# Optimization experiments

Hardware: AMD Instinct MI355X
Metric: run time of the kernel (lower is better)

Reference implementation:

```python
import jax, jax.numpy as jnp
import numpy as np

N_NODES = 20000
N_EDGES = 640000
IN_DIM = 256
HID = 128
N_GRAPHS = 64


def setup_inputs() -> dict:
    key = jax.random.key(0)
    ks = jax.random.split(key, 9)
    x = jax.random.normal(ks[0], (N_NODES, IN_DIM), jnp.float32)
    edge_index = jax.random.randint(ks[1], (2, N_EDGES), 0, N_NODES, dtype=jnp.int32)
    batch = jnp.sort(jax.random.randint(ks[2], (N_NODES,), 0, N_GRAPHS, dtype=jnp.int32))

    def lin(k, fan_in, fan_out):
        # torch.nn.Linear default init: U(-1/sqrt(fan_in), 1/sqrt(fan_in))
        bound = 1.0 / np.sqrt(fan_in)
        kw, kb = jax.random.split(k)
        W = jax.random.uniform(kw, (fan_in, fan_out), jnp.float32, -bound, bound)
        b = jax.random.uniform(kb, (fan_out,), jnp.float32, -bound, bound)
        return W, b

    W0, b0 = lin(ks[3], IN_DIM, HID)
    W1, b1 = lin(ks[4], HID, HID)
    W2, b2 = lin(ks[5], HID, HID)
    return dict(x=x, edge_index=edge_index, batch=batch,
                W0=W0, b0=b0, W1=W1, b1=b1, W2=W2, b2=b2)


def reference(x, edge_index, batch, W0, b0, W1, b1, W2, b2):
    src, dst = edge_index[0], edge_index[1]
    edge_batch = batch[src]  # [E] segment id per edge
    ones = jnp.ones((edge_batch.shape[0], 1), x.dtype)
    counts = jax.ops.segment_sum(ones, edge_batch, num_segments=N_GRAPHS)
    inv_counts = 1.0 / jnp.maximum(counts, 1.0)

    def pool(z):
        # gather endpoint features, concat -> [E, 2*HID], mean pool by graph
        edge_emb = jnp.concatenate([z[src], z[dst]], axis=1)
        return jax.ops.segment_sum(edge_emb, edge_batch, num_segments=N_GRAPHS) * inv_counts

    g = []
    z = x
    for W, b in ((W0, b0), (W1, b1), (W2, b2)):
        z = z @ W + b
        g.append(pool(z))
    return jnp.concatenate(g, axis=1)  # [N_GRAPHS, 3 * 2 * HID]
```

## Files before the change

### kernel.cpp

```cpp
#include <hip/hip_runtime.h>

#define N_NODES 20000
#define N_EDGES 640000
#define N_GRAPHS 64

#define NCHUNK 128
#define CHUNK_SZ 157
#define GSPLIT 8
#define GSUB 8

#define BG_TILE 2048
#define NBG 313
#define SEGCAP 80
#define GR_CAP 768
#define NSLOT4 (NBG * SEGCAP / 4)

#define CD_OFF      0
#define DEG_OFF     1280000
#define CNT_OFF     1300000
#define Y_OFF       1300064
#define PART_OFF    1316448
#define BH_OFF      3413600
#define VALS_OFF    3433632

__global__ __launch_bounds__(256) void bucket_g_k(const int* __restrict__ ei,
                                                  const int* __restrict__ batch,
                                                  unsigned* __restrict__ vals,
                                                  unsigned* __restrict__ bh,
                                                  float* __restrict__ Y) {
    __shared__ unsigned hist[N_GRAPHS];
    __shared__ unsigned base[N_GRAPHS + 1];
    __shared__ unsigned lv[BG_TILE];
    const int t = threadIdx.x;
    const int blk = blockIdx.x;
    if (t < N_GRAPHS) hist[t] = 0u;
    __syncthreads();

    const int e0 = blk * BG_TILE;
    const int ecnt = (e0 + BG_TILE <= N_EDGES) ? BG_TILE : (N_EDGES - e0);
    unsigned pv[8], rnk[8], gg[8];
#pragma unroll
    for (int k = 0; k < 8; ++k) {
        int i = t + k * 256;
        if (i < ecnt) {
            unsigned s = (unsigned)ei[e0 + i];
            unsigned d = (unsigned)ei[N_EDGES + e0 + i];
            unsigned g = (unsigned)batch[s];
            pv[k] = (s << 15) | d;
            gg[k] = g;
            rnk[k] = atomicAdd(&hist[g], 1u);
        } else {
            gg[k] = 0xFFFFFFFFu;
        }
    }
    __syncthreads();
    if (t == 0) {
        unsigned acc = 0u;
        base[0] = 0u;
        for (int g = 0; g < N_GRAPHS; ++g) { acc += hist[g]; base[g + 1] = acc; }
    }
    if (t < N_GRAPHS) {
        unsigned c = hist[t];
        bh[blk * N_GRAPHS + t] = (c > SEGCAP) ? SEGCAP : c;
    }
    __syncthreads();
#pragma unroll
    for (int k = 0; k < 8; ++k) {
        if (gg[k] != 0xFFFFFFFFu) lv[base[gg[k]] + rnk[k]] = pv[k];
    }
    __syncthreads();
    for (int i = t; i < ecnt; i += 256) {
        int lo = 0, hi = N_GRAPHS - 1;
        while (lo < hi) { int m = (lo + hi + 1) >> 1; if (base[m] <= (unsigned)i) lo = m; else hi = m - 1; }
        unsigned slot = (unsigned)i - base[lo];
        if (slot < SEGCAP)
            vals[((size_t)lo * NBG + blk) * SEGCAP + slot] = lv[i];
    }
    if (blk == 0) {
        float4* y4 = (float4*)Y;
        for (int i = t; i < 64 * 64; i += 256) y4[i] = make_float4(0.f, 0.f, 0.f, 0.f);
    }
}

__global__ __launch_bounds__(1024) void cd_col_k(const unsigned* __restrict__ vals,
                                                 const unsigned* __restrict__ bh,
                                                 const int* __restrict__ batch,
                                                 float* __restrict__ Cdcol,
                                                 float* __restrict__ deg,
                                                 float* __restrict__ counts) {
    __shared__ unsigned scnt[NBG];
    __shared__ unsigned dh[2500];
    __shared__ unsigned sdeg[GR_CAP];
    __shared__ int s_lo, s_hi;
    const int t = threadIdx.x;
    const int g = blockIdx.x >> 2;
    const int q = blockIdx.x & 3;
    const int d0 = q * 5000;

    for (int i = t; i < 2500; i += 1024) dh[i] = 0u;
    if (t < NBG) scnt[t] = bh[t * N_GRAPHS + g];
    if (q == 0) {
        if (t < GR_CAP) sdeg[t] = 0u;
        if (t == 0) {
            int lo = 0, hi = N_NODES;
            while (lo < hi) { int m = (lo + hi) >> 1; if (batch[m] < g) lo = m + 1; else hi = m; }
            s_lo = lo;
            int lo2 = lo; hi = N_NODES;
            while (lo2 < hi) { int m = (lo2 + hi) >> 1; if (batch[m] < g + 1) lo2 = m + 1; else hi = m; }
            s_hi = lo2;
        }
    }
    __syncthreads();
    const int lo = (q == 0) ? s_lo : 0;

    const uint4* v4 = (const uint4*)(vals + (size_t)g * NBG * SEGCAP);
    for (int i = t; i < NSLOT4; i += 1024) {
        uint4 v = *(v4 + i);
        unsigned w = (unsigned)i * 4u;
        unsigned seg = (unsigned)(((unsigned long long)w * 53687092ull) >> 32);
        unsigned local = w - seg * 80u;
        unsigned c = scnt[seg];
#define CD_ONE(VX, L)                                                            \
        if ((L) < c) {                                                           \
            int rd_ = (int)((VX) & 0x7FFFu) - d0;                                \
            if ((unsigned)rd_ < 5000u)                                           \
                atomicAdd(&dh[rd_ >> 1], 1u << ((rd_ & 1) * 16));                \
            if (q == 0) {                                                        \
                int rs_ = (int)((VX) >> 15) - lo;                                \
                if ((unsigned)rs_ < (unsigned)GR_CAP) atomicAdd(&sdeg[rs_], 1u); \
            }                                                                    \
        }
        CD_ONE(v.x, local + 0u)
        CD_ONE(v.y, local + 1u)
        CD_ONE(v.z, local + 2u)
        CD_ONE(v.w, local + 3u)
#undef CD_ONE
    }
    __syncthreads();

    float2* outc = (float2*)(Cdcol + (size_t)g * N_NODES + d0);
    for (int w = t; w < 2500; w += 1024) {
        unsigned v = dh[w];
        outc[w] = make_float2((float)(v & 0xFFFFu), (float)(v >> 16));
    }
    if (q == 0) {
        const int range = s_hi - lo;
        for (int i = t; i < range; i += 1024) deg[lo + i] = (float)sdeg[i];
        if (t == 0) {
            unsigned tot = 0;
            for (int i = 0; i < NBG; ++i) tot += scnt[i];
            counts[g] = (float)tot;
        }
    }
}

#define FMA8(C0, C1, XV)                                          \
    acc[0].x = fmaf(C0.x, XV.x, acc[0].x); acc[0].y = fmaf(C0.x, XV.y, acc[0].y); \
    acc[0].z = fmaf(C0.x, XV.z, acc[0].z); acc[0].w = fmaf(C0.x, XV.w, acc[0].w); \
    acc[1].x = fmaf(C0.y, XV.x, acc[1].x); acc[1].y = fmaf(C0.y, XV.y, acc[1].y); \
    acc[1].z = fmaf(C0.y, XV.z, acc[1].z); acc[1].w = fmaf(C0.y, XV.w, acc[1].w); \
    acc[2].x = fmaf(C0.z, XV.x, acc[2].x); acc[2].y = fmaf(C0.z, XV.y, acc[2].y); \
    acc[2].z = fmaf(C0.z, XV.z, acc[2].z); acc[2].w = fmaf(C0.z, XV.w, acc[2].w); \
    acc[3].x = fmaf(C0.w, XV.x, acc[3].x); acc[3].y = fmaf(C0.w, XV.y, acc[3].y); \
    acc[3].z = fmaf(C0.w, XV.z, acc[3].z); acc[3].w = fmaf(C0.w, XV.w, acc[3].w); \
    acc[4].x = fmaf(C1.x, XV.x, acc[4].x); acc[4].y = fmaf(C1.x, XV.y, acc[4].y); \
    acc[4].z = fmaf(C1.x, XV.z, acc[4].z); acc[4].w = fmaf(C1.x, XV.w, acc[4].w); \
    acc[5].x = fmaf(C1.y, XV.x, acc[5].x); acc[5].y = fmaf(C1.y, XV.y, acc[5].y); \
    acc[5].z = fmaf(C1.y, XV.z, acc[5].z); acc[5].w = fmaf(C1.y, XV.w, acc[5].w); \
    acc[6].x = fmaf(C1.z, XV.x, acc[6].x); acc[6].y = fmaf(C1.z, XV.y, acc[6].y); \
    acc[6].z = fmaf(C1.z, XV.z, acc[6].z); acc[6].w = fmaf(C1.z, XV.w, acc[6].w); \
    acc[7].x = fmaf(C1.w, XV.x, acc[7].x); acc[7].y = fmaf(C1.w, XV.y, acc[7].y); \
    acc[7].z = fmaf(C1.w, XV.z, acc[7].z); acc[7].w = fmaf(C1.w, XV.w, acc[7].w);

__global__ __launch_bounds__(256) void pool_k(const float* __restrict__ x,
                                              const int* __restrict__ batch,
                                              const float* __restrict__ Cdcol,
                                              const float* __restrict__ deg,
                                              float* __restrict__ Y,
                                              float* __restrict__ part) {
    __shared__ float4 sc4[CHUNK_SZ * 2];
    __shared__ float sdeg[CHUNK_SZ];
    __shared__ int   sbatch[CHUNK_SZ];
    __shared__ float4 red[2 * GSUB * 64];

    const int t = threadIdx.x;
    const int fg = t & 63;
    const int p  = t >> 6;
    const int b = blockIdx.x & 127;
    const int j = blockIdx.x >> 7;
    const int n0 = b * CHUNK_SZ;
    const int cnt = (n0 + CHUNK_SZ <= N_NODES) ? CHUNK_SZ : (N_NODES - n0);

    float* sc = (float*)sc4;
    const float* cbase = Cdcol + (size_t)(j * GSUB) * N_NODES + n0;
#pragma unroll
    for (int k = 0; k < GSUB; ++k)
        for (int i = t; i < cnt; i += 256)
            sc[i * GSUB + k] = cbase[(size_t)k * N_NODES + i];
    if (j == 0) {
        for (int i = t; i < cnt; i += 256) {
            sdeg[i] = deg[n0 + i];
            sbatch[i] = batch[n0 + i];
        }
    }
    __syncthreads();

    const float4* xp = (const float4*)x + (size_t)n0 * 64 + fg;
#define XL(I) xp[(size_t)(I) * 64]
    float4 acc[GSUB];
#pragma unroll
    for (int k = 0; k < GSUB; ++k) acc[k] = make_float4(0.f, 0.f, 0.f, 0.f);

    if (j == 0) {
        float4 accs = make_float4(0.f, 0.f, 0.f, 0.f);
        int gprev = (p < cnt) ? sbatch[p] : 0;
        int i = p;
        float4 xn = make_float4(0.f, 0.f, 0.f, 0.f);
        if (i < cnt) xn = XL(i);
        for (; i < cnt; i += 4) {
            float4 xv = xn;
            if (i + 4 < cnt) xn = XL(i + 4);
            int g = sbatch[i];
            if (g != gprev) {
                float* yr = Y + gprev * 256 + fg * 4;
                atomicAdd(yr + 0, accs.x); atomicAdd(yr + 1, accs.y);
                atomicAdd(yr + 2, accs.z); atomicAdd(yr + 3, accs.w);
                accs = make_float4(0.f, 0.f, 0.f, 0.f);
                gprev = g;
            }
            float dg = sdeg[i];
            accs.x = fmaf(dg, xv.x, accs.x); accs.y = fmaf(dg, xv.y, accs.y);
            accs.z = fmaf(dg, xv.z, accs.z); accs.w = fmaf(dg, xv.w, accs.w);
            float4 c0 = sc4[i * 2], c1 = sc4[i * 2 + 1];
            FMA8(c0, c1, xv)
        }
        if (p < cnt) {
            float* yr = Y + gprev * 256 + fg * 4;
            atomicAdd(yr + 0, accs.x); atomicAdd(yr + 1, accs.y);
            atomicAdd(yr + 2, accs.z); atomicAdd(yr + 3, accs.w);
        }
    } else {
        int i = p;
        float4 xa, xb, xc, xd;
        if (i      < cnt) xa = XL(i);
        if (i + 4  < cnt) xb = XL(i + 4);
        if (i + 8  < cnt) xc = XL(i + 8);
        if (i + 12 < cnt) xd = XL(i + 12);
        for (; i + 12 < cnt; i += 16) {
            float4 y0 = xa, y1 = xb, y2 = xc, y3 = xd;
            if (i + 16 < cnt) xa = XL(i + 16);
            if (i + 20 < cnt) xb = XL(i + 20);
            if (i + 24 < cnt) xc = XL(i + 24);
            if (i + 28 < cnt) xd = XL(i + 28);
            {
                float4 c0 = sc4[i * 2], c1 = sc4[i * 2 + 1];
                FMA8(c0, c1, y0)
            }
            {
                float4 c0 = sc4[(i + 4) * 2], c1 = sc4[(i + 4) * 2 + 1];
                FMA8(c0, c1, y1)
            }
            {
                float4 c0 = sc4[(i + 8) * 2], c1 = sc4[(i + 8) * 2 + 1];
                FMA8(c0, c1, y2)
            }
            {
                float4 c0 = sc4[(i + 12) * 2], c1 = sc4[(i + 12) * 2 + 1];
                FMA8(c0, c1, y3)
            }
        }
        for (; i < cnt; i += 4) {
            float4 xv = XL(i);
            float4 c0 = sc4[i * 2], c1 = sc4[i * 2 + 1];
            FMA8(c0, c1, xv)
        }
    }
#undef XL

    if (p >= 2) {
#pragma unroll
        for (int k = 0; k < GSUB; ++k) red[(p - 2) * (GSUB * 64) + k * 64 + fg] = acc[k];
    }
    __syncthreads();
    if (p < 2) {
#pragma unroll
        for (int k = 0; k < GSUB; ++k) {
            float4 v = red[p * (GSUB * 64) + k * 64 + fg];
            acc[k].x += v.x; acc[k].y += v.y; acc[k].z += v.z; acc[k].w += v.w;
        }
    }
    __syncthreads();
    if (p == 1) {
#pragma unroll
        for (int k = 0; k < GSUB; ++k) red[k * 64 + fg] = acc[k];
    }
    __syncthreads();
    if (p == 0) {
        float4* part4 = (float4*)part;
#pragma unroll
        for (int k = 0; k < GSUB; ++k) {
            float4 v = red[k * 64 + fg];
            acc[k].x += v.x; acc[k].y += v.y; acc[k].z += v.z; acc[k].w += v.w;
            part4[(size_t)(b * 64 + j * GSUB + k) * 64 + fg] = acc[k];
        }
    }
}

__global__ __launch_bounds__(256) void chain2_k(const float* __restrict__ Y,
                                                const float* __restrict__ part,
                                                const float* __restrict__ counts,
                                                const float* __restrict__ W0, const float* __restrict__ b0,
                                                const float* __restrict__ W1, const float* __restrict__ b1,
                                                const float* __restrict__ W2, const float* __restrict__ b2,
                                                float* __restrict__ out) {
    __shared__ float m[256];
    __shared__ float h[128];
    const int r = blockIdx.x;
    const int t = threadIdx.x;
    const int g = r & 63;
    const int half = (r >= 64) ? 128 : 0;

    float c = counts[g];
    float inv = 1.0f / fmaxf(c, 1.0f);
    float beta = c * inv;

    if (r < 64) {
        m[t] = Y[r * 256 + t] * inv;
    } else {
        float s = 0.0f;
        for (int bb = 0; bb < NCHUNK; ++bb) s += part[(size_t)(bb * 64 + g) * 256 + t];
        m[t] = s * inv;
    }
    __syncthreads();

    if (t < 128) {
        float s1 = 0.0f;
        for (int k = 0; k < 256; ++k) s1 += m[k] * W0[k * 128 + t];
        s1 += beta * b0[t];
        out[g * 768 + 0 + half + t] = s1;
        h[t] = s1;
    }
    __syncthreads();
    float s2 = 0.0f;
    if (t < 128) {
        for (int k = 0; k < 128; ++k) s2 += h[k] * W1[k * 128 + t];
        s2 += beta * b1[t];
        out[g * 768 + 256 + half + t] = s2;
    }
    __syncthreads();
    if (t < 128) h[t] = s2;
    __syncthreads();
    if (t < 128) {
        float s3 = 0.0f;
        for (int k = 0; k < 128; ++k) s3 += h[k] * W2[k * 128 + t];
        s3 += beta * b2[t];
        out[g * 768 + 512 + half + t] = s3;
    }
}

extern "C" void kernel_launch(void* const* d_in, const int* in_sizes, int n_in,
                              void* d_out, int out_size, void* d_ws, size_t ws_size,
                              hipStream_t stream) {
    const float* x     = (const float*)d_in[0];
    const int*   ei    = (const int*)d_in[1];
    const int*   batch = (const int*)d_in[2];
    const float* W0    = (const float*)d_in[3];
    const float* b0    = (const float*)d_in[4];
    const float* W1    = (const float*)d_in[5];
    const float* b1    = (const float*)d_in[6];
    const float* W2    = (const float*)d_in[7];
    const float* b2    = (const float*)d_in[8];
    float* out = (float*)d_out;

    float*    ws     = (float*)d_ws;
    float*    Cdcol  = ws + CD_OFF;
    float*    deg    = ws + DEG_OFF;
    float*    counts = ws + CNT_OFF;
    float*    Y      = ws + Y_OFF;
    float*    part   = ws + PART_OFF;
    unsigned* bh     = (unsigned*)(ws + BH_OFF);
    unsigned* vals   = (unsigned*)(ws + VALS_OFF);

    bucket_g_k<<<NBG, 256, 0, stream>>>(ei, batch, vals, bh, Y);
    cd_col_k<<<N_GRAPHS * 4, 1024, 0, stream>>>(vals, bh, batch, Cdcol, deg, counts);
    pool_k<<<NCHUNK * GSPLIT, 256, 0, stream>>>(x, batch, Cdcol, deg, Y, part);
    chain2_k<<<128, 256, 0, stream>>>(Y, part, counts, W0, b0, W1, b1, W2, b2, out);
}
```

Before: 127.7 us.

## Halve per-block graph subset in pool kernel and replace binary search with lookup table

```diff
diff --git a/kernel.cpp b/kernel.cpp
--- a/kernel.cpp
+++ b/kernel.cpp
@@ -6,8 +6,8 @@
 
 #define NCHUNK 128
 #define CHUNK_SZ 157
-#define GSPLIT 8
-#define GSUB 8
+#define GSPLIT 16
+#define GSUB 4
 
 #define BG_TILE 2048
 #define NBG 313
@@ -31,6 +31,7 @@
     __shared__ unsigned hist[N_GRAPHS];
     __shared__ unsigned base[N_GRAPHS + 1];
     __shared__ unsigned lv[BG_TILE];
+    __shared__ unsigned char gidx[BG_TILE];
     const int t = threadIdx.x;
     const int blk = blockIdx.x;
     if (t < N_GRAPHS) hist[t] = 0u;
@@ -64,17 +65,20 @@
         bh[blk * N_GRAPHS + t] = (c > SEGCAP) ? SEGCAP : c;
     }
     __syncthreads();
+    if (t < N_GRAPHS) {
+        unsigned b0 = base[t], b1 = base[t + 1];
+        for (unsigned i = b0; i < b1; ++i) gidx[i] = (unsigned char)t;
+    }
 #pragma unroll
     for (int k = 0; k < 8; ++k) {
         if (gg[k] != 0xFFFFFFFFu) lv[base[gg[k]] + rnk[k]] = pv[k];
     }
     __syncthreads();
     for (int i = t; i < ecnt; i += 256) {
-        int lo = 0, hi = N_GRAPHS - 1;
-        while (lo < hi) { int m = (lo + hi + 1) >> 1; if (base[m] <= (unsigned)i) lo = m; else hi = m - 1; }
-        unsigned slot = (unsigned)i - base[lo];
+        unsigned g = gidx[i];
+        unsigned slot = (unsigned)i - base[g];
         if (slot < SEGCAP)
-            vals[((size_t)lo * NBG + blk) * SEGCAP + slot] = lv[i];
+            vals[((size_t)g * NBG + blk) * SEGCAP + slot] = lv[i];
     }
     if (blk == 0) {
         float4* y4 = (float4*)Y;
@@ -154,7 +158,7 @@
     }
 }
 
-#define FMA8(C0, C1, XV)                                          \
+#define FMA4(C0, XV)                                              \
     acc[0].x = fmaf(C0.x, XV.x, acc[0].x); acc[0].y = fmaf(C0.x, XV.y, acc[0].y); \
     acc[0].z = fmaf(C0.x, XV.z, acc[0].z); acc[0].w = fmaf(C0.x, XV.w, acc[0].w); \
     acc[1].x = fmaf(C0.y, XV.x, acc[1].x); acc[1].y = fmaf(C0.y, XV.y, acc[1].y); \
@@ -162,23 +166,15 @@
     acc[2].x = fmaf(C0.z, XV.x, acc[2].x); acc[2].y = fmaf(C0.z, XV.y, acc[2].y); \
     acc[2].z = fmaf(C0.z, XV.z, acc[2].z); acc[2].w = fmaf(C0.z, XV.w, acc[2].w); \
     acc[3].x = fmaf(C0.w, XV.x, acc[3].x); acc[3].y = fmaf(C0.w, XV.y, acc[3].y); \
-    acc[3].z = fmaf(C0.w, XV.z, acc[3].z); acc[3].w = fmaf(C0.w, XV.w, acc[3].w); \
-    acc[4].x = fmaf(C1.x, XV.x, acc[4].x); acc[4].y = fmaf(C1.x, XV.y, acc[4].y); \
-    acc[4].z = fmaf(C1.x, XV.z, acc[4].z); acc[4].w = fmaf(C1.x, XV.w, acc[4].w); \
-    acc[5].x = fmaf(C1.y, XV.x, acc[5].x); acc[5].y = fmaf(C1.y, XV.y, acc[5].y); \
-    acc[5].z = fmaf(C1.y, XV.z, acc[5].z); acc[5].w = fmaf(C1.y, XV.w, acc[5].w); \
-    acc[6].x = fmaf(C1.z, XV.x, acc[6].x); acc[6].y = fmaf(C1.z, XV.y, acc[6].y); \
-    acc[6].z = fmaf(C1.z, XV.z, acc[6].z); acc[6].w = fmaf(C1.z, XV.w, acc[6].w); \
-    acc[7].x = fmaf(C1.w, XV.x, acc[7].x); acc[7].y = fmaf(C1.w, XV.y, acc[7].y); \
-    acc[7].z = fmaf(C1.w, XV.z, acc[7].z); acc[7].w = fmaf(C1.w, XV.w, acc[7].w);
-
-__global__ __launch_bounds__(256) void pool_k(const float* __restrict__ x,
-                                              const int* __restrict__ batch,
-                                              const float* __restrict__ Cdcol,
-                                              const float* __restrict__ deg,
-                                              float* __restrict__ Y,
-                                              float* __restrict__ part) {
-    __shared__ float4 sc4[CHUNK_SZ * 2];
+    acc[3].z = fmaf(C0.w, XV.z, acc[3].z); acc[3].w = fmaf(C0.w, XV.w, acc[3].w);
+
+__global__ __launch_bounds__(256, 8) void pool_k(const float* __restrict__ x,
+                                                 const int* __restrict__ batch,
+                                                 const float* __restrict__ Cdcol,
+                                                 const float* __restrict__ deg,
+                                                 float* __restrict__ Y,
+                                                 float* __restrict__ part) {
+    __shared__ float4 sc4[CHUNK_SZ];
     __shared__ float sdeg[CHUNK_SZ];
     __shared__ int   sbatch[CHUNK_SZ];
     __shared__ float4 red[2 * GSUB * 64];
@@ -231,8 +227,8 @@
             float dg = sdeg[i];
             accs.x = fmaf(dg, xv.x, accs.x); accs.y = fmaf(dg, xv.y, accs.y);
             accs.z = fmaf(dg, xv.z, accs.z); accs.w = fmaf(dg, xv.w, accs.w);
-            float4 c0 = sc4[i * 2], c1 = sc4[i * 2 + 1];
-            FMA8(c0, c1, xv)
+            float4 c0 = sc4[i];
+            FMA4(c0, xv)
         }
         if (p < cnt) {
             float* yr = Y + gprev * 256 + fg * 4;
@@ -252,27 +248,15 @@
             if (i + 20 < cnt) xb = XL(i + 20);
             if (i + 24 < cnt) xc = XL(i + 24);
             if (i + 28 < cnt) xd = XL(i + 28);
-            {
-                float4 c0 = sc4[i * 2], c1 = sc4[i * 2 + 1];
-                FMA8(c0, c1, y0)
-            }
-            {
-                float4 c0 = sc4[(i + 4) * 2], c1 = sc4[(i + 4) * 2 + 1];
-                FMA8(c0, c1, y1)
-            }
-            {
-                float4 c0 = sc4[(i + 8) * 2], c1 = sc4[(i + 8) * 2 + 1];
-                FMA8(c0, c1, y2)
-            }
-            {
-                float4 c0 = sc4[(i + 12) * 2], c1 = sc4[(i + 12) * 2 + 1];
-                FMA8(c0, c1, y3)
-            }
+            { float4 c0 = sc4[i];      FMA4(c0, y0) }
+            { float4 c0 = sc4[i + 4];  FMA4(c0, y1) }
+            { float4 c0 = sc4[i + 8];  FMA4(c0, y2) }
+            { float4 c0 = sc4[i + 12]; FMA4(c0, y3) }
         }
         for (; i < cnt; i += 4) {
             float4 xv = XL(i);
-            float4 c0 = sc4[i * 2], c1 = sc4[i * 2 + 1];
-            FMA8(c0, c1, xv)
+            float4 c0 = sc4[i];
+            FMA4(c0, xv)
         }
     }
 #undef XL
```

Measured after the change: 131.8 us. +3.2%, slower.

## Double pool chunk count, shrink prefetch depth, replace bucket binary search with lookup

Applied to the files above, without the earlier changes.

```diff
diff --git a/kernel.cpp b/kernel.cpp
--- a/kernel.cpp
+++ b/kernel.cpp
@@ -4,8 +4,8 @@
 #define N_EDGES 640000
 #define N_GRAPHS 64
 
-#define NCHUNK 128
-#define CHUNK_SZ 157
+#define NCHUNK 256
+#define CHUNK_SZ 79
 #define GSPLIT 8
 #define GSUB 8
 
@@ -20,8 +20,8 @@
 #define CNT_OFF     1300000
 #define Y_OFF       1300064
 #define PART_OFF    1316448
-#define BH_OFF      3413600
-#define VALS_OFF    3433632
+#define BH_OFF      5510752
+#define VALS_OFF    5530784
 
 __global__ __launch_bounds__(256) void bucket_g_k(const int* __restrict__ ei,
                                                   const int* __restrict__ batch,
@@ -31,6 +31,7 @@
     __shared__ unsigned hist[N_GRAPHS];
     __shared__ unsigned base[N_GRAPHS + 1];
     __shared__ unsigned lv[BG_TILE];
+    __shared__ unsigned char gidx[BG_TILE];
     const int t = threadIdx.x;
     const int blk = blockIdx.x;
     if (t < N_GRAPHS) hist[t] = 0u;
@@ -64,17 +65,20 @@
         bh[blk * N_GRAPHS + t] = (c > SEGCAP) ? SEGCAP : c;
     }
     __syncthreads();
+    if (t < N_GRAPHS) {
+        unsigned b0 = base[t], b1 = base[t + 1];
+        for (unsigned i = b0; i < b1; ++i) gidx[i] = (unsigned char)t;
+    }
 #pragma unroll
     for (int k = 0; k < 8; ++k) {
         if (gg[k] != 0xFFFFFFFFu) lv[base[gg[k]] + rnk[k]] = pv[k];
     }
     __syncthreads();
     for (int i = t; i < ecnt; i += 256) {
-        int lo = 0, hi = N_GRAPHS - 1;
-        while (lo < hi) { int m = (lo + hi + 1) >> 1; if (base[m] <= (unsigned)i) lo = m; else hi = m - 1; }
-        unsigned slot = (unsigned)i - base[lo];
+        unsigned g = gidx[i];
+        unsigned slot = (unsigned)i - base[g];
         if (slot < SEGCAP)
-            vals[((size_t)lo * NBG + blk) * SEGCAP + slot] = lv[i];
+            vals[((size_t)g * NBG + blk) * SEGCAP + slot] = lv[i];
     }
     if (blk == 0) {
         float4* y4 = (float4*)Y;
@@ -186,10 +190,12 @@
     const int t = threadIdx.x;
     const int fg = t & 63;
     const int p  = t >> 6;
-    const int b = blockIdx.x & 127;
-    const int j = blockIdx.x >> 7;
+    const int b = blockIdx.x & 255;
+    const int j = blockIdx.x >> 8;
     const int n0 = b * CHUNK_SZ;
-    const int cnt = (n0 + CHUNK_SZ <= N_NODES) ? CHUNK_SZ : (N_NODES - n0);
+    int cnt = N_NODES - n0;
+    if (cnt > CHUNK_SZ) cnt = CHUNK_SZ;
+    if (cnt < 0) cnt = 0;
 
     float* sc = (float*)sc4;
     const float* cbase = Cdcol + (size_t)(j * GSUB) * N_NODES + n0;
@@ -241,33 +247,15 @@
         }
     } else {
         int i = p;
-        float4 xa, xb, xc, xd;
-        if (i      < cnt) xa = XL(i);
-        if (i + 4  < cnt) xb = XL(i + 4);
-        if (i + 8  < cnt) xc = XL(i + 8);
-        if (i + 12 < cnt) xd = XL(i + 12);
-        for (; i + 12 < cnt; i += 16) {
-            float4 y0 = xa, y1 = xb, y2 = xc, y3 = xd;
-            if (i + 16 < cnt) xa = XL(i + 16);
-            if (i + 20 < cnt) xb = XL(i + 20);
-            if (i + 24 < cnt) xc = XL(i + 24);
-            if (i + 28 < cnt) xd = XL(i + 28);
-            {
-                float4 c0 = sc4[i * 2], c1 = sc4[i * 2 + 1];
-                FMA8(c0, c1, y0)
-            }
-            {
-                float4 c0 = sc4[(i + 4) * 2], c1 = sc4[(i + 4) * 2 + 1];
-                FMA8(c0, c1, y1)
-            }
-            {
-                float4 c0 = sc4[(i + 8) * 2], c1 = sc4[(i + 8) * 2 + 1];
-                FMA8(c0, c1, y2)
-            }
-            {
-                float4 c0 = sc4[(i + 12) * 2], c1 = sc4[(i + 12) * 2 + 1];
-                FMA8(c0, c1, y3)
-            }
+        float4 xa, xb;
+        if (i     < cnt) xa = XL(i);
+        if (i + 4 < cnt) xb = XL(i + 4);
+        for (; i + 4 < cnt; i += 8) {
+            float4 y0 = xa, y1 = xb;
+            if (i + 8  < cnt) xa = XL(i + 8);
+            if (i + 12 < cnt) xb = XL(i + 12);
+            { float4 c0 = sc4[i * 2],       c1 = sc4[i * 2 + 1];       FMA8(c0, c1, y0) }
+            { float4 c0 = sc4[(i + 4) * 2], c1 = sc4[(i + 4) * 2 + 1]; FMA8(c0, c1, y1) }
         }
         for (; i < cnt; i += 4) {
             float4 xv = XL(i);
```

Result: no change. 130.0 us (+1.9%).
